# Optimization experiments

Measured on AMD Instinct MI355X. Metric: run time of the kernel, lower is better.

Reference implementation:

```python
import jax, jax.numpy as jnp
import numpy as np

NEG_INF = -1e9  # fp32-safe mask value for non-edges
ALPHA = 0.2     # LeakyReLU negative slope


def setup_inputs() -> dict:
    key = jax.random.key(0)
    k1, k2, k3, k4, k5 = jax.random.split(key, 5)
    N, F_in, H, F_out = 4096, 512, 8, 64
    features = jax.random.normal(k1, (N, F_in), dtype=jnp.float32)
    adjacency_matrix = jax.random.randint(k2, (N, N), 0, 2, dtype=jnp.int32)
    W = jax.random.normal(k3, (H, F_in, F_out), dtype=jnp.float32) * (F_in ** -0.5)
    a_src = jax.random.normal(k4, (H, F_out), dtype=jnp.float32) * (F_out ** -0.5)
    a_dst = jax.random.normal(k5, (H, F_out), dtype=jnp.float32) * (F_out ** -0.5)
    return {"features": features, "adjacency_matrix": adjacency_matrix,
            "W": W, "a_src": a_src, "a_dst": a_dst}


def reference(features, adjacency_matrix, W, a_src, a_dst):
    # Per-head linear projection: [H, N, F_out]
    Wh = jnp.einsum('nf,hfo->hno', features, W)
    # Attention logits e_ij = LeakyReLU(a_src . Wh_i + a_dst . Wh_j)
    src = jnp.einsum('hno,ho->hn', Wh, a_src)  # [H, N]
    dst = jnp.einsum('hno,ho->hn', Wh, a_dst)  # [H, N]
    e = jax.nn.leaky_relu(src[:, :, None] + dst[:, None, :], ALPHA)  # [H, N, N]
    mask = (adjacency_matrix > 0)[None, :, :]
    e = jnp.where(mask, e, jnp.asarray(NEG_INF, e.dtype))
    attn = jax.nn.softmax(e, axis=-1)  # adjacency-masked row softmax
    h = jnp.einsum('hij,hjo->hio', attn, Wh)  # [H, N, F_out]
    h = jax.nn.elu(h)
    # concat=True: torch.cat over feature dim -> [N, H*F_out]
    return jnp.transpose(h, (1, 0, 2)).reshape(h.shape[1], -1)
```

## Files before the change

kernel.cpp:

```cpp
#include <hip/hip_runtime.h>
#include <hip/hip_bf16.h>

typedef __bf16 bf16x8 __attribute__((ext_vector_type(8)));
typedef _Float16 f16x8 __attribute__((ext_vector_type(8)));
typedef _Float16 f16x2 __attribute__((ext_vector_type(2)));
typedef float  f32x4  __attribute__((ext_vector_type(4)));
typedef unsigned short u16x8 __attribute__((ext_vector_type(8)));
typedef unsigned short us4   __attribute__((ext_vector_type(4)));

#define HH    8
#define NN    4096
#define FIN   512
#define FOUT  64
#define ALPHA 0.2f

__global__ __launch_bounds__(256) void k_transpose_w(
    const float* __restrict__ Wsrc, __hip_bfloat16* __restrict__ WT) {
    __shared__ __hip_bfloat16 lt[64][65];
    const int h  = blockIdx.x >> 3;
    const int f0 = (blockIdx.x & 7) * 64;
    const int tid = threadIdx.x;
#pragma unroll
    for (int p = 0; p < 16; ++p) {
        int f = p * 4 + (tid >> 6);
        int o = tid & 63;
        lt[f][o] = __float2bfloat16(Wsrc[((size_t)h * FIN + f0 + f) * FOUT + o]);
    }
    __syncthreads();
#pragma unroll
    for (int p = 0; p < 16; ++p) {
        int o = p * 4 + (tid >> 6);
        int f = tid & 63;
        WT[((size_t)h * FOUT + o) * FIN + f0 + f] = lt[f][o];
    }
}

__global__ __launch_bounds__(256) void k_prep(
    const int* __restrict__ adj,
    unsigned* __restrict__ maskdst, int mstride,
    const float* __restrict__ feat,
    const __hip_bfloat16* __restrict__ WT,
    const float* __restrict__ a_src,
    const float* __restrict__ a_dst,
    unsigned short* __restrict__ WhT,
    float* __restrict__ srcv,
    unsigned short* __restrict__ Ebf, unsigned short* __restrict__ Fbf) {
    __shared__ alignas(16) __hip_bfloat16 lfeat[32][520];

    const int tid = threadIdx.x;

    if (blockIdx.x < 2048) {
        const size_t base = (size_t)blockIdx.x * 8192;
        unsigned m = 0;
#pragma unroll
        for (int p = 0; p < 8; ++p) {
            int4 v = *(const int4*)(adj + base + tid * 32 + p * 4);
            m |= (unsigned)(v.x > 0) << (p * 4);
            m |= (unsigned)(v.y > 0) << (p * 4 + 1);
            m |= (unsigned)(v.z > 0) << (p * 4 + 2);
            m |= (unsigned)(v.w > 0) << (p * 4 + 3);
        }
        __syncthreads();
        maskdst[(size_t)blockIdx.x * mstride + tid] = m;
        return;
    }

    const int pb   = blockIdx.x - 2048;
    const int tile = pb & 127;
    const int hgy  = pb >> 7;

#pragma unroll
    for (int p = 0; p < 16; ++p) {
        int idx  = p * 256 + tid;
        int row  = idx >> 7;
        int col4 = (idx & 127) * 4;
        float4 f = *(const float4*)(feat + (size_t)(tile * 32 + row) * FIN + col4);
        __hip_bfloat16* dst = &lfeat[row][col4];
        dst[0] = __float2bfloat16(f.x); dst[1] = __float2bfloat16(f.y);
        dst[2] = __float2bfloat16(f.z); dst[3] = __float2bfloat16(f.w);
    }
    __syncthreads();

    const int h     = hgy * 4 + (tid >> 6);
    const int lane  = tid & 63;
    const int row16 = lane & 15;
    const int quad  = lane >> 4;

    const unsigned short* WTu = (const unsigned short*)WT + (size_t)h * FOUT * FIN;

    f32x4 acc[2][4] = {};
    for (int k0 = 0; k0 < FIN; k0 += 32) {
        bf16x8 a0 = *(const bf16x8*)&lfeat[row16][k0 + quad * 8];
        bf16x8 a1 = *(const bf16x8*)&lfeat[16 + row16][k0 + quad * 8];
#pragma unroll
        for (int ot = 0; ot < 4; ++ot) {
            bf16x8 b = *(const bf16x8*)(WTu + (size_t)(ot * 16 + row16) * FIN + k0 + quad * 8);
            acc[0][ot] = __builtin_amdgcn_mfma_f32_16x16x32_bf16(a0, b, acc[0][ot], 0, 0, 0);
            acc[1][ot] = __builtin_amdgcn_mfma_f32_16x16x32_bf16(a1, b, acc[1][ot], 0, 0, 0);
        }
    }

#pragma unroll
    for (int g = 0; g < 2; ++g)
#pragma unroll
        for (int ot = 0; ot < 4; ++ot) {
            us4 u;
#pragma unroll
            for (int r = 0; r < 4; ++r)
                u[r] = __builtin_bit_cast(unsigned short, (_Float16)acc[g][ot][r]);
            *(us4*)(WhT + (size_t)(h * FOUT + ot * 16 + row16) * NN
                        + tile * 32 + g * 16 + quad * 4) = u;
        }

    float asv[4], adv[4];
#pragma unroll
    for (int ot = 0; ot < 4; ++ot) {
        asv[ot] = a_src[h * FOUT + ot * 16 + row16];
        adv[ot] = a_dst[h * FOUT + ot * 16 + row16];
    }
#pragma unroll
    for (int g = 0; g < 2; ++g)
#pragma unroll
        for (int r = 0; r < 4; ++r) {
            float ss = 0.f, dd = 0.f;
#pragma unroll
            for (int ot = 0; ot < 4; ++ot) {
                ss += acc[g][ot][r] * asv[ot];
                dd += acc[g][ot][r] * adv[ot];
            }
            ss += __shfl_xor(ss, 1); ss += __shfl_xor(ss, 2);
            ss += __shfl_xor(ss, 4); ss += __shfl_xor(ss, 8);
            dd += __shfl_xor(dd, 1); dd += __shfl_xor(dd, 2);
            dd += __shfl_xor(dd, 4); dd += __shfl_xor(dd, 8);
            if (row16 == 0) {
                int n = tile * 32 + g * 16 + quad * 4 + r;
                srcv[h * NN + n] = ss;
                _Float16 e = (_Float16)__expf(dd);
                _Float16 f = (_Float16)__expf(ALPHA * dd);
                Ebf[h * NN + n] = __builtin_bit_cast(unsigned short, e);
                Fbf[h * NN + n] = __builtin_bit_cast(unsigned short, f);
            }
        }
}

__global__ __launch_bounds__(256, 3) void k_flash(
    const unsigned* __restrict__ maskp, int mstride,
    const float* __restrict__ srcv,
    const unsigned short* __restrict__ Ebf,
    const unsigned short* __restrict__ Fbf,
    const unsigned short* __restrict__ WhT,
    float* __restrict__ out) {
    __shared__ float st[2][64 * 68];
    __shared__ float lds_l[2][64];

    unsigned* lmask = (unsigned*)&st[0][0];

    const int tid   = threadIdx.x;
    const int seg   = tid >> 6;
    const int lane  = tid & 63;
    const int row16 = lane & 15;
    const int quad  = lane >> 4;
    const int shl   = quad * 8;
    const int tile  = blockIdx.x;
    const int h     = blockIdx.y;

#pragma unroll
    for (int p = 0; p < 8; ++p) {
        int tt = tid + p * 256;
        int c  = tt >> 6;
        int o  = (tt & 63) * 16;
        int4 v = *(const int4*)((const char*)maskp
                                + ((size_t)(tile * 32 + c) * mstride) * 4 + o);
        int row = c * 2 + (o >> 9);
        int dw  = (o & 511) >> 2;
        *(int4*)&lmask[row * 132 + dw] = v;
    }
    __syncthreads();

    f16x2 Es2[4], Fs2[4];
#pragma unroll
    for (int g = 0; g < 4; ++g) {
        float si = srcv[h * NN + tile * 64 + g * 16 + row16];
        _Float16 e = (_Float16)__expf(si);
        _Float16 f = (_Float16)__expf(ALPHA * si);
        Es2[g][0] = e; Es2[g][1] = e;
        Fs2[g][0] = f; Fs2[g][1] = f;
    }
    const int mbase = row16 * 132 + seg * 32;

    const unsigned short* Eb = Ebf + h * NN + seg * 1024;
    const unsigned short* Fb = Fbf + h * NN + seg * 1024;
    const unsigned short* wh = WhT + (size_t)h * FOUT * NN + seg * 1024;

    f32x4 acc[4][4] = {};
    float lsum[4]   = {};
    const f16x2 ones2 = {(_Float16)1.0f, (_Float16)1.0f};

    int t = (seg * 8) & 31;
    union { f16x8 v8; f16x2 h2[4]; } evu, fvu;
    f16x8 bc[4];
    unsigned mc[4];
    {
        const int jj = t * 32 + shl;
        evu.v8 = *(const f16x8*)(Eb + jj);
        fvu.v8 = *(const f16x8*)(Fb + jj);
#pragma unroll
        for (int ot = 0; ot < 4; ++ot)
            bc[ot] = *(const f16x8*)(wh + (size_t)(ot * 16 + row16) * NN + jj);
#pragma unroll
        for (int g = 0; g < 4; ++g)
            mc[g] = lmask[mbase + g * 2112 + t];
    }

#pragma unroll 1
    for (int i = 0; i < 32; ++i) {
        const int tn = (t + 1) & 31;
        const int jn = tn * 32 + shl;
        union { f16x8 v8; f16x2 h2[4]; } evn, fvn;
        evn.v8 = *(const f16x8*)(Eb + jn);
        fvn.v8 = *(const f16x8*)(Fb + jn);
        f16x8 bn[4];
#pragma unroll
        for (int ot = 0; ot < 4; ++ot)
            bn[ot] = *(const f16x8*)(wh + (size_t)(ot * 16 + row16) * NN + jn);
        unsigned mn[4];
#pragma unroll
        for (int g = 0; g < 4; ++g)
            mn[g] = lmask[mbase + g * 2112 + tn];

#pragma unroll
        for (int g = 0; g < 4; ++g) {
            unsigned mb = mc[g] >> shl;
            union { f16x8 v8; unsigned w[4]; } au;
#pragma unroll
            for (int kk = 0; kk < 4; ++kk) {
                f16x2 t0 = evu.h2[kk] * Es2[g];
                f16x2 t1 = fvu.h2[kk] * Fs2[g];
                f16x2 p2 = __builtin_elementwise_max(t0, t1);
                unsigned lo = (unsigned)__builtin_amdgcn_sbfe((int)mb, 2 * kk, 1);
                unsigned hi = (unsigned)__builtin_amdgcn_sbfe((int)mb, 2 * kk + 1, 1);
                unsigned w  = (lo & 0xFFFFu) | (hi & 0xFFFF0000u);
                unsigned pw = __builtin_bit_cast(unsigned, p2) & w;
                f16x2 mp2   = __builtin_bit_cast(f16x2, pw);
                au.w[kk] = pw;
#if __has_builtin(__builtin_amdgcn_fdot2)
                lsum[g] = __builtin_amdgcn_fdot2(mp2, ones2, lsum[g], false);
#else
                lsum[g] += (float)mp2[0] + (float)mp2[1];
#endif
            }
            __builtin_amdgcn_s_setprio(1);
#pragma unroll
            for (int ot = 0; ot < 4; ++ot)
                acc[g][ot] = __builtin_amdgcn_mfma_f32_16x16x32_f16(au.v8, bc[ot], acc[g][ot], 0, 0, 0);
            __builtin_amdgcn_s_setprio(0);
        }
        evu.v8 = evn.v8;
        fvu.v8 = fvn.v8;
#pragma unroll
        for (int ot = 0; ot < 4; ++ot) bc[ot] = bn[ot];
#pragma unroll
        for (int g = 0; g < 4; ++g) mc[g] = mn[g];
        t = tn;
    }

#pragma unroll
    for (int g = 0; g < 4; ++g) {
        lsum[g] += __shfl_xor(lsum[g], 16);
        lsum[g] += __shfl_xor(lsum[g], 32);
    }

    __syncthreads();

    auto stash = [&](int buf) {
#pragma unroll
        for (int g = 0; g < 4; ++g)
#pragma unroll
            for (int ot = 0; ot < 4; ++ot)
#pragma unroll
                for (int r = 0; r < 4; ++r)
                    st[buf][(g * 16 + quad * 4 + r) * 68 + ot * 16 + row16] = acc[g][ot][r];
        if (quad == 0)
#pragma unroll
            for (int g = 0; g < 4; ++g)
                lds_l[buf][g * 16 + row16] = lsum[g];
    };
    auto addin = [&](int buf) {
#pragma unroll
        for (int g = 0; g < 4; ++g) {
#pragma unroll
            for (int ot = 0; ot < 4; ++ot)
#pragma unroll
                for (int r = 0; r < 4; ++r)
                    acc[g][ot][r] += st[buf][(g * 16 + quad * 4 + r) * 68 + ot * 16 + row16];
            lsum[g] += lds_l[buf][g * 16 + row16];
        }
    };

    if (seg == 1) stash(0);
    if (seg == 3) stash(1);
    __syncthreads();
    if (seg == 0) addin(0);
    if (seg == 2) addin(1);
    __syncthreads();
    if (seg == 2) stash(0);
    __syncthreads();
    if (seg == 0) {
        addin(0);
#pragma unroll
        for (int g = 0; g < 4; ++g)
#pragma unroll
            for (int r = 0; r < 4; ++r) {
                int   qr  = quad * 4 + r;
                float l   = __shfl(lsum[g], qr);
                float rl  = 1.0f / l;
#pragma unroll
                for (int ot = 0; ot < 4; ++ot) {
                    float v = acc[g][ot][r] * rl;
                    float y = v > 0.f ? v : __expf(v) - 1.f;
                    st[0][(g * 16 + qr) * 68 + ot * 16 + row16] = y;
                }
            }
    }
    __syncthreads();
#pragma unroll
    for (int p = 0; p < 4; ++p) {
        int f    = tid + p * 256;
        int row  = f >> 4;
        int col4 = (f & 15) * 4;
        float4 v = *(const float4*)&st[0][row * 68 + col4];
        *(float4*)&out[(size_t)(tile * 64 + row) * (HH * FOUT) + h * FOUT + col4] = v;
    }
}

extern "C" void kernel_launch(void* const* d_in, const int* in_sizes, int n_in,
                              void* d_out, int out_size, void* d_ws, size_t ws_size,
                              hipStream_t stream) {
    const float* features = (const float*)d_in[0];
    int*         adj      = (int*)d_in[1];
    const float* W        = (const float*)d_in[2];
    const float* a_src    = (const float*)d_in[3];
    const float* a_dst    = (const float*)d_in[4];
    float*       out      = (float*)d_out;

    char* ws = (char*)d_ws;
    __hip_bfloat16* WT   = (__hip_bfloat16*)(ws);
    unsigned short* WhT  = (unsigned short*)(ws + (512 << 10));
    float*          srcv = (float*)(ws + (512 << 10) + (4 << 20));
    unsigned short* Ebf  = (unsigned short*)(ws + (512 << 10) + (4 << 20) + (128 << 10));
    unsigned short* Fbf  = (unsigned short*)(ws + (512 << 10) + (4 << 20) + (192 << 10));

    const size_t mask_off = (512 << 10) + (4 << 20) + (256 << 10);
    unsigned* maskp; int mstride;
    if (ws_size >= mask_off + (2u << 20)) {
        maskp   = (unsigned*)(ws + mask_off);
        mstride = 256;
    } else {
        maskp   = (unsigned*)adj;
        mstride = 8192;
    }

    k_transpose_w<<<dim3(64), 256, 0, stream>>>(W, WT);
    k_prep<<<dim3(2048 + 256), 256, 0, stream>>>(adj, maskp, mstride,
                                                 features, WT, a_src, a_dst,
                                                 WhT, srcv, Ebf, Fbf);
    k_flash<<<dim3(64, 8), 256, 0, stream>>>(maskp, mstride, srcv, Ebf, Fbf,
                                             WhT, out);
}
```

Baseline: 164.5 us.

## Tile WhT into contiguous 32-column blocks and double-buffer the attention loop

Changes the WhT storage from row-major [H*F_out][N] to blocked tiles of 64x32 so each 32-column step's B-operand loads come from a contiguous 4KB chunk instead of strided rows. The aggregation loop is restructured into explicit A/B register double buffering, unrolled by two, to remove the register copies between iterations. It also staggers each tile's starting column by tile parity to spread memory accesses. This raises register pressure from the two buffer sets.

New measurement: 153.9 us. -6.4%, faster.

```diff
diff --git a/kernel.cpp b/kernel.cpp
--- a/kernel.cpp
+++ b/kernel.cpp
@@ -108,8 +108,8 @@
 #pragma unroll
             for (int r = 0; r < 4; ++r)
                 u[r] = __builtin_bit_cast(unsigned short, (_Float16)acc[g][ot][r]);
-            *(us4*)(WhT + (size_t)(h * FOUT + ot * 16 + row16) * NN
-                        + tile * 32 + g * 16 + quad * 4) = u;
+            *(us4*)(WhT + (((size_t)(h * 128 + tile) * 64 + ot * 16 + row16) << 5)
+                        + g * 16 + quad * 4) = u;
         }
 
     float asv[4], adv[4];
@@ -188,49 +188,34 @@
     }
     const int mbase = row16 * 132 + seg * 32;
 
-    const unsigned short* Eb = Ebf + h * NN + seg * 1024;
-    const unsigned short* Fb = Fbf + h * NN + seg * 1024;
-    const unsigned short* wh = WhT + (size_t)h * FOUT * NN + seg * 1024;
+    const unsigned short* Eb  = Ebf + h * NN + seg * 1024;
+    const unsigned short* Fb  = Fbf + h * NN + seg * 1024;
+    const unsigned short* whh = WhT + (size_t)h * FOUT * NN;
 
     f32x4 acc[4][4] = {};
     float lsum[4]   = {};
     const f16x2 ones2 = {(_Float16)1.0f, (_Float16)1.0f};
 
-    int t = (seg * 8) & 31;
-    union { f16x8 v8; f16x2 h2[4]; } evu, fvu;
-    f16x8 bc[4];
-    unsigned mc[4];
-    {
-        const int jj = t * 32 + shl;
-        evu.v8 = *(const f16x8*)(Eb + jj);
-        fvu.v8 = *(const f16x8*)(Fb + jj);
+    auto LOAD = [&](f16x8& ev_, f16x8& fv_, f16x8* b_, unsigned* m_, int tt) {
+        const int jj = tt * 32 + shl;
+        const size_t jb = (size_t)(seg * 32 + tt) << 11;
+        ev_ = *(const f16x8*)(Eb + jj);
+        fv_ = *(const f16x8*)(Fb + jj);
 #pragma unroll
         for (int ot = 0; ot < 4; ++ot)
-            bc[ot] = *(const f16x8*)(wh + (size_t)(ot * 16 + row16) * NN + jj);
+            b_[ot] = *(const f16x8*)(whh + jb + (ot * 16 + row16) * 32 + quad * 8);
 #pragma unroll
         for (int g = 0; g < 4; ++g)
-            mc[g] = lmask[mbase + g * 2112 + t];
-    }
-
-#pragma unroll 1
-    for (int i = 0; i < 32; ++i) {
-        const int tn = (t + 1) & 31;
-        const int jn = tn * 32 + shl;
-        union { f16x8 v8; f16x2 h2[4]; } evn, fvn;
-        evn.v8 = *(const f16x8*)(Eb + jn);
-        fvn.v8 = *(const f16x8*)(Fb + jn);
-        f16x8 bn[4];
-#pragma unroll
-        for (int ot = 0; ot < 4; ++ot)
-            bn[ot] = *(const f16x8*)(wh + (size_t)(ot * 16 + row16) * NN + jn);
-        unsigned mn[4];
-#pragma unroll
-        for (int g = 0; g < 4; ++g)
-            mn[g] = lmask[mbase + g * 2112 + tn];
-
+            m_[g] = lmask[mbase + g * 2112 + tt];
+    };
+
+    auto COMP = [&](const f16x8& ev_, const f16x8& fv_,
+                    const f16x8* b_, const unsigned* m_) {
+        union { f16x8 v8; f16x2 h2[4]; } evu, fvu;
+        evu.v8 = ev_; fvu.v8 = fv_;
 #pragma unroll
         for (int g = 0; g < 4; ++g) {
-            unsigned mb = mc[g] >> shl;
+            unsigned mb = m_[g] >> shl;
             union { f16x8 v8; unsigned w[4]; } au;
 #pragma unroll
             for (int kk = 0; kk < 4; ++kk) {
@@ -252,16 +237,25 @@
             __builtin_amdgcn_s_setprio(1);
 #pragma unroll
             for (int ot = 0; ot < 4; ++ot)
-                acc[g][ot] = __builtin_amdgcn_mfma_f32_16x16x32_f16(au.v8, bc[ot], acc[g][ot], 0, 0, 0);
+                acc[g][ot] = __builtin_amdgcn_mfma_f32_16x16x32_f16(au.v8, b_[ot], acc[g][ot], 0, 0, 0);
             __builtin_amdgcn_s_setprio(0);
         }
-        evu.v8 = evn.v8;
-        fvu.v8 = fvn.v8;
-#pragma unroll
-        for (int ot = 0; ot < 4; ++ot) bc[ot] = bn[ot];
-#pragma unroll
-        for (int g = 0; g < 4; ++g) mc[g] = mn[g];
-        t = tn;
+    };
+
+    int t0 = ((seg * 8) + ((tile & 1) << 2)) & 31;
+    f16x8 evA, fvA, bA[4]; unsigned mA[4];
+    f16x8 evB, fvB, bB[4]; unsigned mB[4];
+    LOAD(evA, fvA, bA, mA, t0);
+
+#pragma unroll 1
+    for (int i = 0; i < 16; ++i) {
+        const int t1 = (t0 + 1) & 31;
+        LOAD(evB, fvB, bB, mB, t1);
+        COMP(evA, fvA, bA, mA);
+        const int t2 = (t0 + 2) & 31;
+        LOAD(evA, fvA, bA, mA, t2);
+        COMP(evB, fvB, bB, mB);
+        t0 = t2;
     }
 
 #pragma unroll
```
